# Kernel optimization log

Measured on AMD Instinct MI355X. Metric: run time of the kernel, lower is better.

The kernel has to match this reference:

```python
import jax, jax.numpy as jnp
import numpy as np

B, C, N, T = 16, 32, 300, 12
ST, DH, CO = 40, 16, 32
DY_INTERVAL = 3
GDEP = 2
ALPHA = 0.05


def setup_inputs() -> dict:
    key = jax.random.key(0)
    ks = jax.random.split(key, 12)
    w = lambda k, shape, s=0.1: (jax.random.normal(k, shape, jnp.float32) * s)
    return {
        "x": jax.random.normal(ks[0], (B, C, N, T), jnp.float32),
        "st_node_fea": jax.random.normal(ks[1], (N, ST), jnp.float32),
        "W_s2d": w(ks[2], (ST, DH)), "b_s2d": jnp.zeros((DH,), jnp.float32),
        "W_rz": w(ks[3], (C + DH, 2 * DH)), "b_rz": jnp.zeros((2 * DH,), jnp.float32),
        "W_h": w(ks[4], (C + DH, DH)), "b_h": jnp.zeros((DH,), jnp.float32),
        "W_c1_fc2": w(ks[5], (2 * DH, DH)), "b_c1_fc2": jnp.zeros((DH,), jnp.float32),
        "W_c1_fc1": w(ks[6], (DH, 1)), "b_c1_fc1": jnp.zeros((1,), jnp.float32),
        "W_c2_fc2": w(ks[7], (2 * DH, DH)), "b_c2_fc2": jnp.zeros((DH,), jnp.float32),
        "W_c2_fc1": w(ks[8], (DH, 1)), "b_c2_fc1": jnp.zeros((1,), jnp.float32),
        "W_mlp": w(ks[9], ((GDEP + 1) * C, CO)), "b_mlp": jnp.zeros((CO,), jnp.float32),
    }


def _edge_score(hs, W_fc2, b_fc2, W_fc1, b_fc1):
    # normal_conv: fc1(relu(fc2(concat([sent, revi], -1)))).
    # fc2 over concat is decomposed into two halves to avoid the [B,N,N,2*DH] concat.
    dh = hs.shape[-1]
    Wa, Wb = W_fc2[:dh], W_fc2[dh:]
    h = jax.nn.relu((hs @ Wa)[:, :, None, :] + (hs @ Wb)[:, None, :, :] + b_fc2)  # [B,N,N,DH]
    return (h @ W_fc1 + b_fc1)[..., 0]  # [B,N,N]


def reference(x, st_node_fea, W_s2d, b_s2d, W_rz, b_rz, W_h, b_h,
              W_c1_fc2, b_c1_fc2, W_c1_fc1, b_c1_fc1,
              W_c2_fc2, b_c2_fc2, W_c2_fc1, b_c2_fc1, W_mlp, b_mlp):
    b, c, n, t = x.shape
    nc = t // DY_INTERVAL
    states0 = jnp.broadcast_to((st_node_fea @ W_s2d + b_s2d)[None], (b, n, DH)) + 0.0
    chunks = jnp.moveaxis(x.reshape(b, c, n, nc, DY_INTERVAL), 3, 0)  # [nc,B,C,N,di]

    def step(states, x_i):
        # GRU-style dynamic graph learner
        inp = jnp.mean(x_i, axis=-1).transpose(0, 2, 1)  # [B,N,C]
        cat = jnp.concatenate([inp, states], -1)
        rz = jax.nn.sigmoid(cat @ W_rz + b_rz)
        r, z = jnp.split(rz, 2, axis=-1)
        h_ = jnp.tanh(jnp.concatenate([inp, r * states], -1) @ W_h + b_h)
        new_state = z * states + (1.0 - z) * h_
        hs = jax.nn.relu(new_state)  # [B,N,DH]
        support = _edge_score(hs, W_c1_fc2, b_c1_fc2, W_c1_fc1, b_c1_fc1)
        mask = _edge_score(hs, W_c2_fc2, b_c2_fc2, W_c2_fc1, b_c2_fc1)
        adj = support * jax.nn.sigmoid(mask)  # [B,N,N]
        # MixProp multi-hop graph conv
        h = x_i
        outs = [h]
        for _ in range(GDEP):
            h = ALPHA * x_i + (1.0 - ALPHA) * jnp.einsum('bcwt,bvw->bcvt', h, adj)
            outs.append(h)
        ho = jnp.concatenate(outs, axis=1)  # [B,(GDEP+1)*C,N,di]
        out = jnp.einsum('bcnt,co->bont', ho, W_mlp) + b_mlp[None, :, None, None]
        return new_state, out

    _, outs = jax.lax.scan(step, states0, chunks)  # [nc,B,CO,N,di]
    return jnp.moveaxis(outs, 0, 3).reshape(b, W_mlp.shape[1], n, t)
```

## Files before the change

kernel.cpp:

```cpp
#include <hip/hip_runtime.h>
#include <hip/hip_bf16.h>
#include <math.h>

#define BB 16
#define CC 32
#define NN 300
#define TT 12
#define STF 40
#define DHD 16
#define COO 32
#define NCH 4
#define COL 96
#define NIB 64
#define KP  320
#define ALPHAF 0.05f
#define HS 40

typedef __attribute__((ext_vector_type(8))) short short8;
typedef __attribute__((ext_vector_type(4))) float f32x4;
typedef unsigned short ushort_t;

#define O_INP   0
#define O_XVB   614400
#define O_GA1   1536000
#define O_GB1   1843200
#define O_GA2   2150400
#define O_GB2   2457600
#define O_ADJB  2764800
#define O_XTB   6041600
#define O_H1B   7024640
#define O_H1VB  8007680
#define O_WMB   8929280

__device__ __forceinline__ float sigf(float x){ return 1.0f/(1.0f+expf(-x)); }

__global__ void k_prep(const float* __restrict__ x, __hip_bfloat16* __restrict__ xtb,
                       __hip_bfloat16* __restrict__ xvb, float* __restrict__ inp,
                       __hip_bfloat16* __restrict__ h1b, const float* __restrict__ Wm,
                       __hip_bfloat16* __restrict__ Wmb){
    int idx = blockIdx.x*256 + threadIdx.x;
    if (idx >= BB*CC*NN) return;
    if (idx < NIB*COL*(KP-NN)){
        int kk  = idx % (KP-NN);
        int col = (idx / (KP-NN)) % COL;
        int ib  = idx / ((KP-NN)*COL);
        size_t off = ((size_t)ib*COL + col)*KP + NN + kk;
        xtb[off] = __float2bfloat16(0.0f);
        h1b[off] = __float2bfloat16(0.0f);
    }
    if (idx < COO*COL){
        int o = idx / COL, k = idx % COL;
        Wmb[o*COL + k] = __float2bfloat16(Wm[k*COO + o]);
    }
    int n = idx % NN;
    int c = (idx / NN) % CC;
    int b = idx / (NN*CC);
    const float* xp = x + ((b*CC + c)*NN + n)*TT;
    float v[TT];
    #pragma unroll
    for (int t=0;t<TT;t++) v[t] = xp[t];
    #pragma unroll
    for (int i=0;i<NCH;i++){
        float m = (v[3*i]+v[3*i+1]+v[3*i+2])*(1.0f/3.0f);
        int ib = i*BB + b;
        inp[((size_t)ib*NN + n)*CC + c] = m;
        #pragma unroll
        for (int t=0;t<3;t++){
            float val = v[3*i+t];
            int col = c*3 + t;
            xtb[((size_t)ib*COL + col)*KP + n] = __float2bfloat16(val);
            xvb[((size_t)ib*NN + n)*COL + col] = __float2bfloat16(val);
        }
    }
}

__global__ void k_gru_all(const float* __restrict__ stnf, const float* __restrict__ W_s2d,
                          const float* __restrict__ b_s2d, const float* __restrict__ inp,
                          const float* __restrict__ W_rz, const float* __restrict__ b_rz,
                          const float* __restrict__ W_h,  const float* __restrict__ b_h,
                          const float* __restrict__ Wc1,  const float* __restrict__ Wc2,
                          float* __restrict__ ga1, float* __restrict__ gb1,
                          float* __restrict__ ga2, float* __restrict__ gb2){
    int row = blockIdx.x;
    int n   = row % NN;
    int tid = threadIdx.x;
    __shared__ float cat[48];
    __shared__ float r_s[16], z_s[16], hs_s[16], st_s[16];
    if (tid < 16){
        float acc = b_s2d[tid];
        const float* srow = stnf + n*STF;
        #pragma unroll
        for (int k=0;k<STF;k++) acc += srow[k]*W_s2d[k*DHD + tid];
        st_s[tid] = acc;
    }
    __syncthreads();
    for (int i=0;i<NCH;i++){
        const float* ip = inp + ((size_t)i*BB*NN + row)*CC;
        if (tid < CC) cat[tid] = ip[tid];
        else if (tid < 48) cat[tid] = st_s[tid-32];
        __syncthreads();
        if (tid < 32){
            float acc = b_rz[tid];
            #pragma unroll
            for (int k=0;k<48;k++) acc += cat[k]*W_rz[k*32 + tid];
            float s = sigf(acc);
            if (tid < 16) r_s[tid] = s; else z_s[tid-16] = s;
        }
        __syncthreads();
        if (tid < 16) cat[32+tid] = r_s[tid]*st_s[tid];
        __syncthreads();
        if (tid < 16){
            float acc = b_h[tid];
            #pragma unroll
            for (int k=0;k<48;k++) acc += cat[k]*W_h[k*DHD + tid];
            float h_ = tanhf(acc);
            float z  = z_s[tid];
            float ns = z*st_s[tid] + (1.0f-z)*h_;
            st_s[tid] = ns;
            hs_s[tid] = fmaxf(ns, 0.0f);
        }
        __syncthreads();
        int j = tid & 15, which = tid >> 4;
        const float* W = (which < 2) ? Wc1 : Wc2;
        int off = (which & 1) ? 16*DHD : 0;
        float acc = 0.0f;
        #pragma unroll
        for (int k=0;k<16;k++) acc += hs_s[k]*W[off + k*DHD + j];
        float* dst = (which==0)? ga1 : (which==1)? gb1 : (which==2)? ga2 : gb2;
        dst[((size_t)i*BB*NN + row)*DHD + j] = acc;
        __syncthreads();
    }
}

#define AVT 8
__global__ void k_adj(const float* __restrict__ ga1, const float* __restrict__ gb1,
                      const float* __restrict__ ga2, const float* __restrict__ gb2,
                      const float* __restrict__ bfc2_1, const float* __restrict__ wfc1_1, const float* __restrict__ bfc1_1,
                      const float* __restrict__ bfc2_2, const float* __restrict__ wfc1_2, const float* __restrict__ bfc1_2,
                      __hip_bfloat16* __restrict__ adjb){
    int tile = blockIdx.x % 38;
    int ib   = blockIdx.x / 38;
    int v0 = tile * AVT;
    int tid = threadIdx.x;
    __shared__ float a1[AVT][16], a2[AVT][16];
    __shared__ float w1[16], w2[16];
    if (tid < 16) w1[tid] = wfc1_1[tid];
    else if (tid < 32) w2[tid-16] = wfc1_2[tid-16];
    {
        int vl = tid >> 5, which = (tid >> 4) & 1, k = tid & 15;
        int v = v0 + vl;
        float val = 0.0f;
        if (v < NN)
            val = which ? (ga2[((size_t)ib*NN+v)*DHD + k] + bfc2_2[k])
                        : (ga1[((size_t)ib*NN+v)*DHD + k] + bfc2_1[k]);
        if (which) a2[vl][k] = val; else a1[vl][k] = val;
    }
    float B1 = bfc1_1[0], B2 = bfc1_2[0];
    __syncthreads();
    for (int w = tid; w < KP; w += 256){
        if (w < NN){
            const float4* p1 = (const float4*)(gb1 + ((size_t)ib*NN + w)*DHD);
            const float4* p2 = (const float4*)(gb2 + ((size_t)ib*NN + w)*DHD);
            float4 A[4], Bv[4];
            #pragma unroll
            for (int q=0;q<4;q++){ A[q]=p1[q]; Bv[q]=p2[q]; }
            const float* g1 = (const float*)A;
            const float* g2 = (const float*)Bv;
            for (int vl=0; vl<AVT; vl++){
                if (v0+vl >= NN) break;
                float s = B1, m = B2;
                #pragma unroll
                for (int k=0;k<16;k++){
                    s += fmaxf(a1[vl][k] + g1[k], 0.0f)*w1[k];
                    m += fmaxf(a2[vl][k] + g2[k], 0.0f)*w2[k];
                }
                adjb[((size_t)ib*KP + v0+vl)*KP + w] = __float2bfloat16(s * sigf(m));
            }
        } else {
            for (int vl=0; vl<AVT; vl++){
                if (v0+vl >= NN) break;
                adjb[((size_t)ib*KP + v0+vl)*KP + w] = __float2bfloat16(0.0f);
            }
        }
    }
}

__device__ __forceinline__ void conv_mfma_tile(const __hip_bfloat16* __restrict__ adjb,
                                               const __hip_bfloat16* __restrict__ Hb,
                                               int ib, int v0, int wave, int lane,
                                               f32x4& acc0, f32x4& acc1, f32x4& acc2){
    int l15 = lane & 15, lk = lane >> 4;
    int wrow = (wave & 1) * 16;
    int wcol = (wave >> 1) * 48;
    const short8* Ap  = (const short8*)(adjb + ((size_t)ib*KP + v0 + wrow + l15)*KP + 8*lk);
    const short8* Bp0 = (const short8*)(Hb   + ((size_t)ib*COL + wcol +  0 + l15)*KP + 8*lk);
    const short8* Bp1 = (const short8*)(Hb   + ((size_t)ib*COL + wcol + 16 + l15)*KP + 8*lk);
    const short8* Bp2 = (const short8*)(Hb   + ((size_t)ib*COL + wcol + 32 + l15)*KP + 8*lk);
    #pragma unroll 2
    for (int kk=0; kk<KP/32; kk++){
        short8 a = Ap[kk*4];
        acc0 = __builtin_amdgcn_mfma_f32_16x16x32_bf16(a, Bp0[kk*4], acc0, 0, 0, 0);
        acc1 = __builtin_amdgcn_mfma_f32_16x16x32_bf16(a, Bp1[kk*4], acc1, 0, 0, 0);
        acc2 = __builtin_amdgcn_mfma_f32_16x16x32_bf16(a, Bp2[kk*4], acc2, 0, 0, 0);
    }
}

__global__ __launch_bounds__(256) void k_conv1(const __hip_bfloat16* __restrict__ adjb,
                                               const __hip_bfloat16* __restrict__ xtb,
                                               const __hip_bfloat16* __restrict__ xvb,
                                               __hip_bfloat16* __restrict__ h1b,
                                               __hip_bfloat16* __restrict__ h1vb){
    int ib = blockIdx.x / 10;
    int v0 = (blockIdx.x % 10) * 32;
    int tid = threadIdx.x;
    int wave = tid >> 6, lane = tid & 63;
    int l15 = lane & 15, lk = lane >> 4;
    int wrow = (wave & 1) * 16;
    int wcol = (wave >> 1) * 48;
    __shared__ float hbuf[COL][33];
    f32x4 acc0 = {0.f,0.f,0.f,0.f}, acc1 = acc0, acc2 = acc0;
    conv_mfma_tile(adjb, xtb, ib, v0, wave, lane, acc0, acc1, acc2);
    f32x4 accs[3] = {acc0, acc1, acc2};
    #pragma unroll
    for (int t=0;t<3;t++){
        int col = wcol + t*16 + l15;
        #pragma unroll
        for (int r=0;r<4;r++){
            int vloc = wrow + lk*4 + r;
            int v = v0 + vloc;
            float xval = (v < NN) ? __bfloat162float(xvb[((size_t)ib*NN + v)*COL + col]) : 0.0f;
            hbuf[col][vloc] = ALPHAF*xval + (1.0f-ALPHAF)*accs[t][r];
        }
    }
    __syncthreads();
    for (int idx = tid; idx < COL*32; idx += 256){
        int col = idx >> 5, vloc = idx & 31;
        int v = v0 + vloc;
        if (v < NN)
            h1b[((size_t)ib*COL + col)*KP + v] = __float2bfloat16(hbuf[col][vloc]);
    }
    for (int idx = tid; idx < 32*COL; idx += 256){
        int vloc = idx / COL, col = idx % COL;
        int v = v0 + vloc;
        if (v < NN)
            h1vb[((size_t)ib*NN + v)*COL + col] = __float2bfloat16(hbuf[col][vloc]);
    }
}

__global__ __launch_bounds__(256) void k_conv2_mlp(const __hip_bfloat16* __restrict__ adjb,
                                                   const __hip_bfloat16* __restrict__ h1b,
                                                   const __hip_bfloat16* __restrict__ xvb,
                                                   const __hip_bfloat16* __restrict__ h1vb,
                                                   const __hip_bfloat16* __restrict__ Wmb,
                                                   const float* __restrict__ bmlp,
                                                   float* __restrict__ out){
    int ib = blockIdx.x / 10;
    int v0 = (blockIdx.x % 10) * 32;
    int b  = ib % BB, chunk = ib / BB;
    int tid = threadIdx.x;
    int wave = tid >> 6, lane = tid & 63;
    int l15 = lane & 15, lk = lane >> 4;
    int wrow = (wave & 1) * 16;
    int wcol = (wave >> 1) * 48;
    __shared__ ushort_t hst[3][3][32][HS];
    for (int idx = tid; idx < 2*32*COL; idx += 256){
        int which = idx / (32*COL);
        int r     = idx % (32*COL);
        int vloc  = r / COL, col = r % COL;
        int v = v0 + vloc;
        int c = col/3, t = col%3;
        ushort_t val = 0;
        if (v < NN){
            const ushort_t* src = (const ushort_t*)(which ? h1vb : xvb);
            val = src[((size_t)ib*NN + v)*COL + col];
        }
        hst[t][which][vloc][c] = val;
    }
    f32x4 acc0 = {0.f,0.f,0.f,0.f}, acc1 = acc0, acc2 = acc0;
    conv_mfma_tile(adjb, h1b, ib, v0, wave, lane, acc0, acc1, acc2);
    f32x4 accs[3] = {acc0, acc1, acc2};
    #pragma unroll
    for (int tt=0;tt<3;tt++){
        int col = wcol + tt*16 + l15;
        int c = col/3, t = col%3;
        #pragma unroll
        for (int r=0;r<4;r++){
            int vloc = wrow + lk*4 + r;
            int v = v0 + vloc;
            float val = 0.0f;
            if (v < NN){
                float xval = __bfloat162float(xvb[((size_t)ib*NN + v)*COL + col]);
                val = ALPHAF*xval + (1.0f-ALPHAF)*accs[tt][r];
            }
            __hip_bfloat16 bv = __float2bfloat16(val);
            hst[t][2][vloc][c] = *(ushort_t*)&bv;
        }
    }
    __syncthreads();
    #pragma unroll
    for (int j=0;j<3;j++){
        int tile = wave + 4*j;
        int t  = tile >> 2;
        int vt = (tile & 3) >> 1;
        int ot = tile & 1;
        f32x4 acc = {0.f,0.f,0.f,0.f};
        #pragma unroll
        for (int d=0;d<3;d++){
            short8 a = *(const short8*)&hst[t][d][vt*16 + l15][8*lk];
            short8 bfr = *(const short8*)(Wmb + ((size_t)(ot*16 + l15))*COL + d*32 + 8*lk);
            acc = __builtin_amdgcn_mfma_f32_16x16x32_bf16(a, bfr, acc, 0, 0, 0);
        }
        int o = ot*16 + l15;
        float bias = bmlp[o];
        #pragma unroll
        for (int r=0;r<4;r++){
            int v = v0 + vt*16 + lk*4 + r;
            if (v < NN)
                out[(((size_t)b*COO + o)*NN + v)*TT + chunk*3 + t] = acc[r] + bias;
        }
    }
}

extern "C" void kernel_launch(void* const* d_in, const int* in_sizes, int n_in,
                              void* d_out, int out_size, void* d_ws, size_t ws_size,
                              hipStream_t stream){
    const float* x     = (const float*)d_in[0];
    const float* stnf  = (const float*)d_in[1];
    const float* W_s2d = (const float*)d_in[2];
    const float* b_s2d = (const float*)d_in[3];
    const float* W_rz  = (const float*)d_in[4];
    const float* b_rz  = (const float*)d_in[5];
    const float* W_h   = (const float*)d_in[6];
    const float* b_h   = (const float*)d_in[7];
    const float* Wc1f2 = (const float*)d_in[8];
    const float* bc1f2 = (const float*)d_in[9];
    const float* Wc1f1 = (const float*)d_in[10];
    const float* bc1f1 = (const float*)d_in[11];
    const float* Wc2f2 = (const float*)d_in[12];
    const float* bc2f2 = (const float*)d_in[13];
    const float* Wc2f1 = (const float*)d_in[14];
    const float* bc2f1 = (const float*)d_in[15];
    const float* W_mlp = (const float*)d_in[16];
    const float* b_mlp = (const float*)d_in[17];
    float* out = (float*)d_out;
    float* ws  = (float*)d_ws;

    float* inp = ws + O_INP;
    float* ga1 = ws + O_GA1;
    float* gb1 = ws + O_GB1;
    float* ga2 = ws + O_GA2;
    float* gb2 = ws + O_GB2;
    __hip_bfloat16* xvb  = (__hip_bfloat16*)(ws + O_XVB);
    __hip_bfloat16* adjb = (__hip_bfloat16*)(ws + O_ADJB);
    __hip_bfloat16* xtb  = (__hip_bfloat16*)(ws + O_XTB);
    __hip_bfloat16* h1b  = (__hip_bfloat16*)(ws + O_H1B);
    __hip_bfloat16* h1vb = (__hip_bfloat16*)(ws + O_H1VB);
    __hip_bfloat16* Wmb  = (__hip_bfloat16*)(ws + O_WMB);

    hipLaunchKernelGGL(k_prep, dim3(600), dim3(256), 0, stream, x, xtb, xvb, inp, h1b, W_mlp, Wmb);
    hipLaunchKernelGGL(k_gru_all, dim3(BB*NN), dim3(64), 0, stream,
                       stnf, W_s2d, b_s2d, inp, W_rz, b_rz, W_h, b_h, Wc1f2, Wc2f2,
                       ga1, gb1, ga2, gb2);
    hipLaunchKernelGGL(k_adj, dim3(NIB*38), dim3(256), 0, stream,
                       ga1, gb1, ga2, gb2,
                       bc1f2, Wc1f1, bc1f1, bc2f2, Wc2f1, bc2f1, adjb);
    hipLaunchKernelGGL(k_conv1, dim3(NIB*10), dim3(256), 0, stream,
                       adjb, xtb, xvb, h1b, h1vb);
    hipLaunchKernelGGL(k_conv2_mlp, dim3(NIB*10), dim3(256), 0, stream,
                       adjb, h1b, xvb, h1vb, Wmb, b_mlp, out);
}
```

Before: 223.5 us.

## Hoist GRU input projection into parallel kernel and use wave shuffles in recurrence

The input-dependent part of the GRU gate and candidate matmuls moves into a new fully parallel kernel, `k_iproj`, which writes `irz` and `ih` to workspace. The recurrent kernel then keeps its state-side weights in registers and exchanges values with wavefront shuffles instead of shared memory and repeated `__syncthreads`. This shortens the serial per-chunk dependency chain. The adjacency kernel now covers the full padded row range of 320 and writes explicit zeros for rows at or past 300, and its row loop is unrolled. The cost is one more launch and some extra workspace traffic.

```diff
diff --git a/kernel.cpp b/kernel.cpp
--- a/kernel.cpp
+++ b/kernel.cpp
@@ -15,6 +15,7 @@
 #define KP  320
 #define ALPHAF 0.05f
 #define HS 40
+#define ATILES 40
 
 typedef __attribute__((ext_vector_type(8))) short short8;
 typedef __attribute__((ext_vector_type(4))) float f32x4;
@@ -31,6 +32,8 @@
 #define O_H1B   7024640
 #define O_H1VB  8007680
 #define O_WMB   8929280
+#define O_IRZ   8932352
+#define O_IH    9546752
 
 __device__ __forceinline__ float sigf(float x){ return 1.0f/(1.0f+expf(-x)); }
 
@@ -74,75 +77,110 @@
     }
 }
 
-__global__ void k_gru_all(const float* __restrict__ stnf, const float* __restrict__ W_s2d,
-                          const float* __restrict__ b_s2d, const float* __restrict__ inp,
-                          const float* __restrict__ W_rz, const float* __restrict__ b_rz,
-                          const float* __restrict__ W_h,  const float* __restrict__ b_h,
-                          const float* __restrict__ Wc1,  const float* __restrict__ Wc2,
-                          float* __restrict__ ga1, float* __restrict__ gb1,
-                          float* __restrict__ ga2, float* __restrict__ gb2){
+__global__ void k_iproj(const float* __restrict__ inp,
+                        const float* __restrict__ W_rz, const float* __restrict__ b_rz,
+                        const float* __restrict__ W_h,  const float* __restrict__ b_h,
+                        float* __restrict__ irz, float* __restrict__ ih){
+    int idx = blockIdx.x*256 + threadIdx.x;
+    if (idx >= NCH*BB*NN*48) return;
+    int j    = idx % 48;
+    int rowg = idx / 48;
+    const float* ip = inp + (size_t)rowg*CC;
+    float a0=0.f,a1=0.f,a2=0.f,a3=0.f;
+    if (j < 32){
+        #pragma unroll
+        for (int k=0;k<32;k+=4){
+            a0 += ip[k  ]*W_rz[(k  )*32+j];
+            a1 += ip[k+1]*W_rz[(k+1)*32+j];
+            a2 += ip[k+2]*W_rz[(k+2)*32+j];
+            a3 += ip[k+3]*W_rz[(k+3)*32+j];
+        }
+        irz[(size_t)rowg*32 + j] = a0+a1+a2+a3 + b_rz[j];
+    } else {
+        int d = j-32;
+        #pragma unroll
+        for (int k=0;k<32;k+=4){
+            a0 += ip[k  ]*W_h[(k  )*DHD+d];
+            a1 += ip[k+1]*W_h[(k+1)*DHD+d];
+            a2 += ip[k+2]*W_h[(k+2)*DHD+d];
+            a3 += ip[k+3]*W_h[(k+3)*DHD+d];
+        }
+        ih[(size_t)rowg*DHD + d] = a0+a1+a2+a3 + b_h[d];
+    }
+}
+
+__global__ __launch_bounds__(64) void k_gru_all(
+        const float* __restrict__ stnf, const float* __restrict__ W_s2d,
+        const float* __restrict__ b_s2d,
+        const float* __restrict__ irz, const float* __restrict__ ih,
+        const float* __restrict__ W_rz, const float* __restrict__ W_h,
+        const float* __restrict__ Wc1,  const float* __restrict__ Wc2,
+        float* __restrict__ ga1, float* __restrict__ gb1,
+        float* __restrict__ ga2, float* __restrict__ gb2){
     int row = blockIdx.x;
     int n   = row % NN;
     int tid = threadIdx.x;
-    __shared__ float cat[48];
-    __shared__ float r_s[16], z_s[16], hs_s[16], st_s[16];
-    if (tid < 16){
-        float acc = b_s2d[tid];
-        const float* srow = stnf + n*STF;
-        #pragma unroll
-        for (int k=0;k<STF;k++) acc += srow[k]*W_s2d[k*DHD + tid];
-        st_s[tid] = acc;
-    }
-    __syncthreads();
-    for (int i=0;i<NCH;i++){
-        const float* ip = inp + ((size_t)i*BB*NN + row)*CC;
-        if (tid < CC) cat[tid] = ip[tid];
-        else if (tid < 48) cat[tid] = st_s[tid-32];
-        __syncthreads();
-        if (tid < 32){
-            float acc = b_rz[tid];
-            #pragma unroll
-            for (int k=0;k<48;k++) acc += cat[k]*W_rz[k*32 + tid];
-            float s = sigf(acc);
-            if (tid < 16) r_s[tid] = s; else z_s[tid-16] = s;
-        }
-        __syncthreads();
-        if (tid < 16) cat[32+tid] = r_s[tid]*st_s[tid];
-        __syncthreads();
-        if (tid < 16){
-            float acc = b_h[tid];
-            #pragma unroll
-            for (int k=0;k<48;k++) acc += cat[k]*W_h[k*DHD + tid];
-            float h_ = tanhf(acc);
-            float z  = z_s[tid];
-            float ns = z*st_s[tid] + (1.0f-z)*h_;
-            st_s[tid] = ns;
-            hs_s[tid] = fmaxf(ns, 0.0f);
-        }
-        __syncthreads();
-        int j = tid & 15, which = tid >> 4;
+    int d   = tid & 15;
+    float wst[16];
+    if (tid < 32){
+        #pragma unroll
+        for (int k=0;k<16;k++) wst[k] = W_rz[(32+k)*32 + tid];
+    } else if (tid < 48){
+        #pragma unroll
+        for (int k=0;k<16;k++) wst[k] = W_h[(32+k)*DHD + d];
+    } else {
+        #pragma unroll
+        for (int k=0;k<16;k++) wst[k] = 0.0f;
+    }
+    float wpj[16];
+    {
+        int which = tid >> 4;
         const float* W = (which < 2) ? Wc1 : Wc2;
         int off = (which & 1) ? 16*DHD : 0;
-        float acc = 0.0f;
-        #pragma unroll
-        for (int k=0;k<16;k++) acc += hs_s[k]*W[off + k*DHD + j];
+        #pragma unroll
+        for (int k=0;k<16;k++) wpj[k] = W[off + k*DHD + d];
+    }
+    float st = b_s2d[d];
+    {
+        const float* srow = stnf + n*STF;
+        #pragma unroll
+        for (int k=0;k<STF;k++) st += srow[k]*W_s2d[k*DHD + d];
+    }
+    for (int i=0;i<NCH;i++){
+        size_t rowg = (size_t)i*BB*NN + row;
+        float ibase = (tid < 32) ? irz[rowg*32 + tid]
+                    : (tid < 48) ? ih[rowg*DHD + d] : 0.0f;
+        float acc = ibase;
+        #pragma unroll
+        for (int k=0;k<16;k++) acc += __shfl(st, k) * wst[k];
+        float rz = sigf(acc);
+        float acc2 = ibase;
+        #pragma unroll
+        for (int k=0;k<16;k++) acc2 += __shfl(rz, k) * __shfl(st, k) * wst[k];
+        float hh = tanhf(acc2);
+        float z  = __shfl(rz, 16 + d);
+        float hd = __shfl(hh, 32 + d);
+        st = z*st + (1.0f - z)*hd;
+        float hs = fmaxf(st, 0.0f);
+        float acc3 = 0.0f;
+        #pragma unroll
+        for (int k=0;k<16;k++) acc3 += __shfl(hs, k) * wpj[k];
+        int which = tid >> 4;
         float* dst = (which==0)? ga1 : (which==1)? gb1 : (which==2)? ga2 : gb2;
-        dst[((size_t)i*BB*NN + row)*DHD + j] = acc;
-        __syncthreads();
-    }
-}
-
-#define AVT 8
+        dst[rowg*DHD + d] = acc3;
+    }
+}
+
 __global__ void k_adj(const float* __restrict__ ga1, const float* __restrict__ gb1,
                       const float* __restrict__ ga2, const float* __restrict__ gb2,
                       const float* __restrict__ bfc2_1, const float* __restrict__ wfc1_1, const float* __restrict__ bfc1_1,
                       const float* __restrict__ bfc2_2, const float* __restrict__ wfc1_2, const float* __restrict__ bfc1_2,
                       __hip_bfloat16* __restrict__ adjb){
-    int tile = blockIdx.x % 38;
-    int ib   = blockIdx.x / 38;
-    int v0 = tile * AVT;
+    int tile = blockIdx.x % ATILES;
+    int ib   = blockIdx.x / ATILES;
+    int v0 = tile * 8;
     int tid = threadIdx.x;
-    __shared__ float a1[AVT][16], a2[AVT][16];
+    __shared__ float a1[8][16], a2[8][16];
     __shared__ float w1[16], w2[16];
     if (tid < 16) w1[tid] = wfc1_1[tid];
     else if (tid < 32) w2[tid-16] = wfc1_2[tid-16];
@@ -157,6 +195,7 @@
     }
     float B1 = bfc1_1[0], B2 = bfc1_2[0];
     __syncthreads();
+    const __hip_bfloat16 ZB = __float2bfloat16(0.0f);
     for (int w = tid; w < KP; w += 256){
         if (w < NN){
             const float4* p1 = (const float4*)(gb1 + ((size_t)ib*NN + w)*DHD);
@@ -166,20 +205,26 @@
             for (int q=0;q<4;q++){ A[q]=p1[q]; Bv[q]=p2[q]; }
             const float* g1 = (const float*)A;
             const float* g2 = (const float*)Bv;
-            for (int vl=0; vl<AVT; vl++){
-                if (v0+vl >= NN) break;
-                float s = B1, m = B2;
-                #pragma unroll
-                for (int k=0;k<16;k++){
-                    s += fmaxf(a1[vl][k] + g1[k], 0.0f)*w1[k];
-                    m += fmaxf(a2[vl][k] + g2[k], 0.0f)*w2[k];
+            #pragma unroll
+            for (int vl=0; vl<8; vl++){
+                int v = v0 + vl;
+                if (v < NN){
+                    float s = B1, m = B2;
+                    #pragma unroll
+                    for (int k=0;k<16;k++){
+                        s += fmaxf(a1[vl][k] + g1[k], 0.0f)*w1[k];
+                        m += fmaxf(a2[vl][k] + g2[k], 0.0f)*w2[k];
+                    }
+                    adjb[((size_t)ib*KP + v)*KP + w] = __float2bfloat16(s * sigf(m));
+                } else {
+                    adjb[((size_t)ib*KP + v)*KP + w] = ZB;
                 }
-                adjb[((size_t)ib*KP + v0+vl)*KP + w] = __float2bfloat16(s * sigf(m));
             }
         } else {
-            for (int vl=0; vl<AVT; vl++){
-                if (v0+vl >= NN) break;
-                adjb[((size_t)ib*KP + v0+vl)*KP + w] = __float2bfloat16(0.0f);
+            #pragma unroll
+            for (int vl=0; vl<8; vl++){
+                int v = v0 + vl;
+                adjb[((size_t)ib*KP + v)*KP + w] = ZB;
             }
         }
     }
@@ -350,6 +395,8 @@
     float* gb1 = ws + O_GB1;
     float* ga2 = ws + O_GA2;
     float* gb2 = ws + O_GB2;
+    float* irz = ws + O_IRZ;
+    float* ih  = ws + O_IH;
     __hip_bfloat16* xvb  = (__hip_bfloat16*)(ws + O_XVB);
     __hip_bfloat16* adjb = (__hip_bfloat16*)(ws + O_ADJB);
     __hip_bfloat16* xtb  = (__hip_bfloat16*)(ws + O_XTB);
@@ -358,10 +405,12 @@
     __hip_bfloat16* Wmb  = (__hip_bfloat16*)(ws + O_WMB);
 
     hipLaunchKernelGGL(k_prep, dim3(600), dim3(256), 0, stream, x, xtb, xvb, inp, h1b, W_mlp, Wmb);
+    hipLaunchKernelGGL(k_iproj, dim3(3600), dim3(256), 0, stream,
+                       inp, W_rz, b_rz, W_h, b_h, irz, ih);
     hipLaunchKernelGGL(k_gru_all, dim3(BB*NN), dim3(64), 0, stream,
-                       stnf, W_s2d, b_s2d, inp, W_rz, b_rz, W_h, b_h, Wc1f2, Wc2f2,
+                       stnf, W_s2d, b_s2d, irz, ih, W_rz, W_h, Wc1f2, Wc2f2,
                        ga1, gb1, ga2, gb2);
-    hipLaunchKernelGGL(k_adj, dim3(NIB*38), dim3(256), 0, stream,
+    hipLaunchKernelGGL(k_adj, dim3(NIB*ATILES), dim3(256), 0, stream,
                        ga1, gb1, ga2, gb2,
                        bc1f2, Wc1f1, bc1f1, bc2f2, Wc2f1, bc2f1, adjb);
     hipLaunchKernelGGL(k_conv1, dim3(NIB*10), dim3(256), 0, stream,
```

After: 345.7 us. 54.7% more time.
